# Optimization experiments

Hardware: AMD Instinct MI355X
Metric: run time of the kernel (lower is better)

## Reference

```python
import jax, jax.numpy as jnp
import numpy as np

ALPHA = 8.3  # depth-similarity decay from Depth-aware CNN
K = 3        # kernel size
PAD = 1      # padding (stride=1, dilation=1)


def _patches(x, k, pad):
    """Extract kxk stride-1 patches. x: (B,C,H,W) -> (B,C,k,k,H,W)."""
    B, C, H, W = x.shape
    xp = jnp.pad(x, ((0, 0), (0, 0), (pad, pad), (pad, pad)))
    rows = []
    for i in range(k):
        cols = [xp[:, :, i:i + H, j:j + W] for j in range(k)]
        rows.append(jnp.stack(cols, axis=2))          # (B,C,k,H,W)
    return jnp.stack(rows, axis=2)                     # (B,C,k,k,H,W)


def setup_inputs() -> dict:
    key = jax.random.key(0)
    k1, k2, k3 = jax.random.split(key, 3)
    B, Cin, H, W = 8, 512, 64, 64
    Cout = 64
    x = jax.random.normal(k1, (B, Cin, H, W), dtype=jnp.float32)
    depth = jax.random.uniform(k2, (B, 1, H, W), dtype=jnp.float32)
    stdv = 1.0 / np.sqrt(Cin * K * K)
    weight = jax.random.uniform(k3, (Cout, Cin, K, K), dtype=jnp.float32,
                                minval=-stdv, maxval=stdv)
    return {"input": x, "depth": depth, "weight": weight}


def reference(input, depth, weight):
    # depth-modulated conv: out(p0) = sum_pn w(pn) * x(p0+pn) * exp(-a*|d(p0)-d(p0+pn)|)
    xpat = _patches(input, K, PAD)                 # (B,Cin,K,K,H,W)
    dpat = _patches(depth, K, PAD)                 # (B,1,K,K,H,W)
    d0 = depth[:, :, None, None, :, :]             # center depth (B,1,1,1,H,W)
    gate = jnp.exp(-ALPHA * jnp.abs(d0 - dpat))    # (B,1,K,K,H,W)
    out = jnp.einsum('ocij,bcijhw->bohw', weight, xpat * gate)
    return out
```

## Files before the change

### kernel.cpp

```cpp
#include <hip/hip_runtime.h>
#include <math.h>

#define ALPHA 8.3f
#define XSZ   16896
#define WSZ   36864
#define BUFSZ 53760

typedef short v8s  __attribute__((ext_vector_type(8)));
typedef float v16f __attribute__((ext_vector_type(16)));
typedef float v4f  __attribute__((ext_vector_type(4)));

static __device__ __forceinline__ unsigned short f2bf(float f) {
    unsigned int u = __float_as_uint(f);
    u = (u + 0x7fffu + ((u >> 16) & 1u)) >> 16;
    return (unsigned short)u;
}

static __device__ __forceinline__ void async16(const void* g, void* l) {
    __builtin_amdgcn_global_load_lds(
        (const __attribute__((address_space(1))) unsigned int*)g,
        (__attribute__((address_space(3))) unsigned int*)l, 16, 0, 0);
}

__global__ __launch_bounds__(256) void prep_weights(const float* __restrict__ w,
                                                    unsigned short* __restrict__ wt) {
    const int i = blockIdx.x * 256 + threadIdx.x;
    if (i >= 294912) return;
    const int j    = i & 7;
    const int lane = (i >> 3) & 63;
    const int F    = i >> 9;
    const int kc   = F & 1;
    const int mt   = (F >> 1) & 1;
    const int tq   = F >> 2;
    const int tap  = tq % 9;
    const int ss   = tq / 9;
    const int o    = mt * 32 + (lane & 31);
    const int cin  = ss * 32 + kc * 16 + (lane >> 5) * 8 + j;
    wt[i] = f2bf(w[(o * 512 + cin) * 9 + tap]);
}

__global__ __launch_bounds__(384, 2)
void depthconv_v17(const float* __restrict__ x,
                   const float* __restrict__ depth,
                   const unsigned short* __restrict__ wt,
                   float* __restrict__ out) {
    __shared__ __align__(16) char smem[2 * BUFSZ];

    const int bx   = blockIdx.x;
    const int xcd  = bx & 7;
    const int i0   = bx >> 3;
    const int b    = i0 & 7;
    const int h0   = (xcd * 4 + (i0 >> 3)) * 2;

    const int tid  = threadIdx.x;
    const int wid  = tid >> 6;
    const int lane = tid & 63;
    const int l31  = lane & 31;
    const int half = lane >> 5;
    const int rt   = wid & 1;
    const int di   = wid >> 1;

    const float* xb = x + (size_t)b * 2097152;
    const float* xsrc[3];
    int  goff[3];
    bool gval[3], gact[3];
#pragma unroll
    for (int it = 0; it < 3; ++it) {
        const int g_i = it * 384 + tid;
        const bool act = (g_i < 1056);
        const int p_ = g_i / 264;
        const int s_ = g_i - p_ * 264;
        const int r_ = s_ / 66, c_ = s_ - r_ * 66;
        const int hh = h0 - 1 + r_, ww = c_ - 1;
        const bool val = act && hh >= 0 && hh < 64 && ww >= 0 && ww < 64;
        gact[it] = act;
        gval[it] = val;
        goff[it] = g_i * 16;
        xsrc[it] = val ? (xb + (size_t)(p_ * 8) * 4096 + hh * 64 + ww) : xb;
    }

#define XLOAD(SS, V)                                                             \
    {                                                                            \
        const size_t adv = (size_t)(SS) * 131072;       \
        _Pragma("unroll")                                                        \
        for (int it = 0; it < 3; ++it)                                           \
            _Pragma("unroll")                                                    \
            for (int e = 0; e < 8; ++e)                                          \
                V[it][e] = gval[it] ? xsrc[it][adv + (size_t)e * 4096] : 0.f;    \
    }
#define XWRITE(V, BSEL)                                                          \
    {                                                                            \
        char* dx = smem + (BSEL) * BUFSZ;                                        \
        _Pragma("unroll")                                                        \
        for (int it = 0; it < 3; ++it)                                           \
            if (gact[it]) {                                                      \
                uint4 u;                                                         \
                u.x = f2bf(V[it][0]) | ((unsigned)f2bf(V[it][1]) << 16);         \
                u.y = f2bf(V[it][2]) | ((unsigned)f2bf(V[it][3]) << 16);         \
                u.z = f2bf(V[it][4]) | ((unsigned)f2bf(V[it][5]) << 16);         \
                u.w = f2bf(V[it][6]) | ((unsigned)f2bf(V[it][7]) << 16);         \
                *(uint4*)(dx + goff[it]) = u;                                    \
            }                                                                    \
    }
#define WISSUE(SS, BSEL)                                                         \
    {                                                                            \
        char* dw = smem + (BSEL) * BUFSZ + XSZ;                                  \
        const char* ws = (const char*)wt + (size_t)(SS) * WSZ;                   \
        _Pragma("unroll")                                                        \
        for (int k = 0; k < 6; ++k)                                              \
            async16(ws + (size_t)(k * 384 + tid) * 16,                           \
                    dw + (k * 384 + tid) * 16);                                  \
    }

    float gt[2][3];
    {
        const float* dp = depth + (size_t)b * 4096;
        const int hq = h0 + rt;
        const int hn = hq + di - 1;
#pragma unroll
        for (int n = 0; n < 2; ++n) {
            const int wq = n * 32 + l31;
            const float d0 = dp[hq * 64 + wq];
#pragma unroll
            for (int dj = 0; dj < 3; ++dj) {
                const int wn = wq + dj - 1;
                const float dn = (hn >= 0 && hn < 64 && wn >= 0 && wn < 64)
                                     ? dp[hn * 64 + wn] : 0.f;
                gt[n][dj] = __expf(-ALPHA * fabsf(d0 - dn));
            }
        }
    }

    v16f a00[3], a01[3], a10[3], a11[3];
#pragma unroll
    for (int d = 0; d < 3; ++d)
#pragma unroll
        for (int r = 0; r < 16; ++r) { a00[d][r] = 0.f; a01[d][r] = 0.f;
                                       a10[d][r] = 0.f; a11[d][r] = 0.f; }

    const int aOff = XSZ + di * 12288 + lane * 16;
    const int bOff = (half * 264 + (rt + di) * 66 + l31) * 16;

    float v[3][8];
    WISSUE(0, 0);
    XLOAD(0, v);
    XWRITE(v, 0);

    for (int ss = 0; ss < 16; ++ss) {
        __syncthreads();
        const int cur = ss & 1;
        const int nxt = cur ^ 1;
        if (ss < 15) {
            WISSUE(ss + 1, nxt);
            XLOAD(ss + 1, v);
        }
        const char* ba = smem + cur * BUFSZ + aOff;
        const char* bb = smem + cur * BUFSZ + bOff;
#pragma unroll
        for (int dj = 0; dj < 3; ++dj) {
#pragma unroll
            for (int kc = 0; kc < 2; ++kc) {
                const v8s w0 = *(const v8s*)(ba + ((dj * 2 + 0) * 2 + kc) * 1024);
                const v8s w1 = *(const v8s*)(ba + ((dj * 2 + 1) * 2 + kc) * 1024);
                const v8s x0 = *(const v8s*)(bb + kc * 8448 + (0 * 32 + dj) * 16);
                const v8s x1 = *(const v8s*)(bb + kc * 8448 + (1 * 32 + dj) * 16);
                a00[dj] = __builtin_amdgcn_mfma_f32_32x32x16_bf16(w0, x0, a00[dj], 0, 0, 0);
                a01[dj] = __builtin_amdgcn_mfma_f32_32x32x16_bf16(w1, x0, a01[dj], 0, 0, 0);
                a10[dj] = __builtin_amdgcn_mfma_f32_32x32x16_bf16(w0, x1, a10[dj], 0, 0, 0);
                a11[dj] = __builtin_amdgcn_mfma_f32_32x32x16_bf16(w1, x1, a11[dj], 0, 0, 0);
            }
        }
        if (ss < 15) XWRITE(v, nxt);
    }

#pragma unroll
    for (int r = 0; r < 16; ++r) {
        a00[0][r] = gt[0][0] * a00[0][r];
        a00[0][r] = fmaf(gt[0][1], a00[1][r], a00[0][r]);
        a00[0][r] = fmaf(gt[0][2], a00[2][r], a00[0][r]);
        a01[0][r] = gt[0][0] * a01[0][r];
        a01[0][r] = fmaf(gt[0][1], a01[1][r], a01[0][r]);
        a01[0][r] = fmaf(gt[0][2], a01[2][r], a01[0][r]);
        a10[0][r] = gt[1][0] * a10[0][r];
        a10[0][r] = fmaf(gt[1][1], a10[1][r], a10[0][r]);
        a10[0][r] = fmaf(gt[1][2], a10[2][r], a10[0][r]);
        a11[0][r] = gt[1][0] * a11[0][r];
        a11[0][r] = fmaf(gt[1][1], a11[1][r], a11[0][r]);
        a11[0][r] = fmaf(gt[1][2], a11[2][r], a11[0][r]);
    }

    __syncthreads();
    float* red = (float*)smem;
    const int rbase = rt * 4096 + lane * 4;
#define EPI_STORE(ACC, N, MT)                                                    \
    _Pragma("unroll")                                                            \
    for (int qd = 0; qd < 4; ++qd) {                                             \
        v4f vv; vv[0] = ACC[0][qd * 4]; vv[1] = ACC[0][qd * 4 + 1];              \
        vv[2] = ACC[0][qd * 4 + 2]; vv[3] = ACC[0][qd * 4 + 3];                  \
        *(v4f*)&red[rbase + ((N) * 2 + (MT)) * 1024 + qd * 256] = vv;            \
    }
#define EPI_ADD(ACC, N, MT)                                                      \
    _Pragma("unroll")                                                            \
    for (int qd = 0; qd < 4; ++qd) {                                             \
        v4f vv = *(const v4f*)&red[rbase + ((N) * 2 + (MT)) * 1024 + qd * 256];  \
        vv[0] += ACC[0][qd * 4];     vv[1] += ACC[0][qd * 4 + 1];                \
        vv[2] += ACC[0][qd * 4 + 2]; vv[3] += ACC[0][qd * 4 + 3];                \
        *(v4f*)&red[rbase + ((N) * 2 + (MT)) * 1024 + qd * 256] = vv;            \
    }
    if (di == 2) {
        EPI_STORE(a00, 0, 0) EPI_STORE(a01, 0, 1) EPI_STORE(a10, 1, 0) EPI_STORE(a11, 1, 1)
    }
    __syncthreads();
    if (di == 1) {
        EPI_ADD(a00, 0, 0) EPI_ADD(a01, 0, 1) EPI_ADD(a10, 1, 0) EPI_ADD(a11, 1, 1)
    }
    __syncthreads();
    if (di == 0) {
        float* ob = out + (size_t)b * 262144 + (h0 + rt) * 64;
#define EPI_OUT(ACC, N, MT)                                                      \
    _Pragma("unroll")                                                            \
    for (int qd = 0; qd < 4; ++qd) {                                             \
        const v4f vv = *(const v4f*)&red[rbase + ((N) * 2 + (MT)) * 1024 + qd * 256]; \
        _Pragma("unroll")                                                        \
        for (int j = 0; j < 4; ++j) {                                            \
            const int rg = qd * 4 + j;                                           \
            const int o = (MT) * 32 + (rg & 3) + 8 * (rg >> 2) + 4 * half;       \
            ob[(size_t)o * 4096 + (N) * 32 + l31] = ACC[0][rg] + vv[j];          \
        }                                                                        \
    }
        EPI_OUT(a00, 0, 0) EPI_OUT(a01, 0, 1) EPI_OUT(a10, 1, 0) EPI_OUT(a11, 1, 1)
    }
}

extern "C" void kernel_launch(void* const* d_in, const int* in_sizes, int n_in,
                              void* d_out, int out_size, void* d_ws, size_t ws_size,
                              hipStream_t stream) {
    const float* x      = (const float*)d_in[0];
    const float* depth  = (const float*)d_in[1];
    const float* weight = (const float*)d_in[2];
    float* out = (float*)d_out;

    unsigned short* wtb = (unsigned short*)d_ws;

    prep_weights<<<1152, 256, 0, stream>>>(weight, wtb);
    depthconv_v17<<<256, 384, 0, stream>>>(x, depth, wtb, out);
}
```

Before: 133.6 us.

## Split output tiles in half width and halve K-chunk for higher occupancy

Each block now covers a 2x32 output tile instead of 2x64, doubling the grid to 512 blocks, and each pipeline stage takes 16 input channels instead of 32, so the loop runs 32 stages. This shrinks LDS buffers and accumulator registers, allowing 3 blocks per CU instead of 2, meant to improve latency hiding and fill the GPU better. In exchange, the x halo and the weights are reloaded by twice as many blocks, there are twice as many barriers, and each stage does fewer MFMAs.

```diff
diff --git a/kernel.cpp b/kernel.cpp
--- a/kernel.cpp
+++ b/kernel.cpp
@@ -2,9 +2,9 @@
 #include <math.h>
 
 #define ALPHA 8.3f
-#define XSZ   16896
-#define WSZ   36864
-#define BUFSZ 53760
+#define XSZ   4352
+#define WSZ   18432
+#define BUFSZ 22784
 
 typedef short v8s  __attribute__((ext_vector_type(8)));
 typedef float v16f __attribute__((ext_vector_type(16)));
@@ -29,18 +29,17 @@
     const int j    = i & 7;
     const int lane = (i >> 3) & 63;
     const int F    = i >> 9;
-    const int kc   = F & 1;
-    const int mt   = (F >> 1) & 1;
-    const int tq   = F >> 2;
-    const int tap  = tq % 9;
-    const int ss   = tq / 9;
+    const int mt   = F & 1;
+    const int t    = F >> 1;
+    const int tap  = t % 9;
+    const int ss   = t / 9;
     const int o    = mt * 32 + (lane & 31);
-    const int cin  = ss * 32 + kc * 16 + (lane >> 5) * 8 + j;
+    const int cin  = ss * 16 + (lane >> 5) * 8 + j;
     wt[i] = f2bf(w[(o * 512 + cin) * 9 + tap]);
 }
 
-__global__ __launch_bounds__(384, 2)
-void depthconv_v17(const float* __restrict__ x,
+__global__ __launch_bounds__(384, 3)
+void depthconv_v18(const float* __restrict__ x,
                    const float* __restrict__ depth,
                    const unsigned short* __restrict__ wt,
                    float* __restrict__ out) {
@@ -49,8 +48,10 @@
     const int bx   = blockIdx.x;
     const int xcd  = bx & 7;
     const int i0   = bx >> 3;
-    const int b    = i0 & 7;
-    const int h0   = (xcd * 4 + (i0 >> 3)) * 2;
+    const int wt2  = i0 & 1;
+    const int b    = (i0 >> 1) & 7;
+    const int ht   = xcd * 4 + (i0 >> 4);
+    const int h0   = ht * 2, w0 = wt2 * 32;
 
     const int tid  = threadIdx.x;
     const int wid  = tid >> 6;
@@ -61,96 +62,82 @@
     const int di   = wid >> 1;
 
     const float* xb = x + (size_t)b * 2097152;
-    const float* xsrc[3];
-    int  goff[3];
-    bool gval[3], gact[3];
-#pragma unroll
-    for (int it = 0; it < 3; ++it) {
-        const int g_i = it * 384 + tid;
-        const bool act = (g_i < 1056);
-        const int p_ = g_i / 264;
-        const int s_ = g_i - p_ * 264;
-        const int r_ = s_ / 66, c_ = s_ - r_ * 66;
-        const int hh = h0 - 1 + r_, ww = c_ - 1;
-        const bool val = act && hh >= 0 && hh < 64 && ww >= 0 && ww < 64;
-        gact[it] = act;
-        gval[it] = val;
-        goff[it] = g_i * 16;
-        xsrc[it] = val ? (xb + (size_t)(p_ * 8) * 4096 + hh * 64 + ww) : xb;
+
+    const bool xact = (tid < 272);
+    bool xval; int goff; const float* xsrc;
+    {
+        const int g  = xact ? tid : 0;
+        const int p_ = (g >= 136) ? 1 : 0;
+        const int s_ = g - p_ * 136;
+        const int r_ = s_ / 34, c_ = s_ - r_ * 34;
+        const int hh = h0 - 1 + r_, ww = w0 - 1 + c_;
+        xval = xact && hh >= 0 && hh < 64 && ww >= 0 && ww < 64;
+        goff = g * 16;
+        xsrc = xval ? (xb + (size_t)(p_ * 8) * 4096 + hh * 64 + ww) : xb;
     }
 
 #define XLOAD(SS, V)                                                             \
     {                                                                            \
-        const size_t adv = (size_t)(SS) * 131072;       \
+        const size_t adv = (size_t)(SS) * 65536;                                 \
         _Pragma("unroll")                                                        \
-        for (int it = 0; it < 3; ++it)                                           \
-            _Pragma("unroll")                                                    \
-            for (int e = 0; e < 8; ++e)                                          \
-                V[it][e] = gval[it] ? xsrc[it][adv + (size_t)e * 4096] : 0.f;    \
+        for (int e = 0; e < 8; ++e)                                              \
+            V[e] = xval ? xsrc[adv + (size_t)e * 4096] : 0.f;                    \
     }
 #define XWRITE(V, BSEL)                                                          \
     {                                                                            \
-        char* dx = smem + (BSEL) * BUFSZ;                                        \
-        _Pragma("unroll")                                                        \
-        for (int it = 0; it < 3; ++it)                                           \
-            if (gact[it]) {                                                      \
-                uint4 u;                                                         \
-                u.x = f2bf(V[it][0]) | ((unsigned)f2bf(V[it][1]) << 16);         \
-                u.y = f2bf(V[it][2]) | ((unsigned)f2bf(V[it][3]) << 16);         \
-                u.z = f2bf(V[it][4]) | ((unsigned)f2bf(V[it][5]) << 16);         \
-                u.w = f2bf(V[it][6]) | ((unsigned)f2bf(V[it][7]) << 16);         \
-                *(uint4*)(dx + goff[it]) = u;                                    \
-            }                                                                    \
+        if (xact) {                                                              \
+            uint4 u;                                                             \
+            u.x = f2bf(V[0]) | ((unsigned)f2bf(V[1]) << 16);                     \
+            u.y = f2bf(V[2]) | ((unsigned)f2bf(V[3]) << 16);                     \
+            u.z = f2bf(V[4]) | ((unsigned)f2bf(V[5]) << 16);                     \
+            u.w = f2bf(V[6]) | ((unsigned)f2bf(V[7]) << 16);                     \
+            *(uint4*)(smem + (BSEL) * BUFSZ + goff) = u;                         \
+        }                                                                        \
     }
 #define WISSUE(SS, BSEL)                                                         \
     {                                                                            \
         char* dw = smem + (BSEL) * BUFSZ + XSZ;                                  \
         const char* ws = (const char*)wt + (size_t)(SS) * WSZ;                   \
         _Pragma("unroll")                                                        \
-        for (int k = 0; k < 6; ++k)                                              \
+        for (int k = 0; k < 3; ++k)                                              \
             async16(ws + (size_t)(k * 384 + tid) * 16,                           \
                     dw + (k * 384 + tid) * 16);                                  \
     }
 
-    float gt[2][3];
+    float gt[3];
     {
         const float* dp = depth + (size_t)b * 4096;
-        const int hq = h0 + rt;
+        const int hq = h0 + rt, wq = w0 + l31;
         const int hn = hq + di - 1;
-#pragma unroll
-        for (int n = 0; n < 2; ++n) {
-            const int wq = n * 32 + l31;
-            const float d0 = dp[hq * 64 + wq];
-#pragma unroll
-            for (int dj = 0; dj < 3; ++dj) {
-                const int wn = wq + dj - 1;
-                const float dn = (hn >= 0 && hn < 64 && wn >= 0 && wn < 64)
-                                     ? dp[hn * 64 + wn] : 0.f;
-                gt[n][dj] = __expf(-ALPHA * fabsf(d0 - dn));
-            }
+        const float d0 = dp[hq * 64 + wq];
+#pragma unroll
+        for (int dj = 0; dj < 3; ++dj) {
+            const int wn = wq + dj - 1;
+            const float dn = (hn >= 0 && hn < 64 && wn >= 0 && wn < 64)
+                                 ? dp[hn * 64 + wn] : 0.f;
+            gt[dj] = __expf(-ALPHA * fabsf(d0 - dn));
         }
     }
 
-    v16f a00[3], a01[3], a10[3], a11[3];
+    v16f am0[3], am1[3];
 #pragma unroll
     for (int d = 0; d < 3; ++d)
 #pragma unroll
-        for (int r = 0; r < 16; ++r) { a00[d][r] = 0.f; a01[d][r] = 0.f;
-                                       a10[d][r] = 0.f; a11[d][r] = 0.f; }
-
-    const int aOff = XSZ + di * 12288 + lane * 16;
-    const int bOff = (half * 264 + (rt + di) * 66 + l31) * 16;
-
-    float v[3][8];
+        for (int r = 0; r < 16; ++r) { am0[d][r] = 0.f; am1[d][r] = 0.f; }
+
+    const int aOff = XSZ + (di * 6) * 1024 + lane * 16;
+    const int bOff = (half * 136 + (rt + di) * 34 + l31) * 16;
+
+    float v[8];
     WISSUE(0, 0);
     XLOAD(0, v);
     XWRITE(v, 0);
 
-    for (int ss = 0; ss < 16; ++ss) {
+    for (int ss = 0; ss < 32; ++ss) {
         __syncthreads();
         const int cur = ss & 1;
         const int nxt = cur ^ 1;
-        if (ss < 15) {
+        if (ss < 31) {
             WISSUE(ss + 1, nxt);
             XLOAD(ss + 1, v);
         }
@@ -158,77 +145,63 @@
         const char* bb = smem + cur * BUFSZ + bOff;
 #pragma unroll
         for (int dj = 0; dj < 3; ++dj) {
-#pragma unroll
-            for (int kc = 0; kc < 2; ++kc) {
-                const v8s w0 = *(const v8s*)(ba + ((dj * 2 + 0) * 2 + kc) * 1024);
-                const v8s w1 = *(const v8s*)(ba + ((dj * 2 + 1) * 2 + kc) * 1024);
-                const v8s x0 = *(const v8s*)(bb + kc * 8448 + (0 * 32 + dj) * 16);
-                const v8s x1 = *(const v8s*)(bb + kc * 8448 + (1 * 32 + dj) * 16);
-                a00[dj] = __builtin_amdgcn_mfma_f32_32x32x16_bf16(w0, x0, a00[dj], 0, 0, 0);
-                a01[dj] = __builtin_amdgcn_mfma_f32_32x32x16_bf16(w1, x0, a01[dj], 0, 0, 0);
-                a10[dj] = __builtin_amdgcn_mfma_f32_32x32x16_bf16(w0, x1, a10[dj], 0, 0, 0);
-                a11[dj] = __builtin_amdgcn_mfma_f32_32x32x16_bf16(w1, x1, a11[dj], 0, 0, 0);
-            }
+            const v8s w0v = *(const v8s*)(ba + (dj * 2 + 0) * 1024);
+            const v8s w1v = *(const v8s*)(ba + (dj * 2 + 1) * 1024);
+            const v8s xv  = *(const v8s*)(bb + dj * 16);
+            am0[dj] = __builtin_amdgcn_mfma_f32_32x32x16_bf16(w0v, xv, am0[dj], 0, 0, 0);
+            am1[dj] = __builtin_amdgcn_mfma_f32_32x32x16_bf16(w1v, xv, am1[dj], 0, 0, 0);
         }
-        if (ss < 15) XWRITE(v, nxt);
-    }
-
+        if (ss < 31) XWRITE(v, nxt);
+    }
+
+    float m0[16], m1[16];
 #pragma unroll
     for (int r = 0; r < 16; ++r) {
-        a00[0][r] = gt[0][0] * a00[0][r];
-        a00[0][r] = fmaf(gt[0][1], a00[1][r], a00[0][r]);
-        a00[0][r] = fmaf(gt[0][2], a00[2][r], a00[0][r]);
-        a01[0][r] = gt[0][0] * a01[0][r];
-        a01[0][r] = fmaf(gt[0][1], a01[1][r], a01[0][r]);
-        a01[0][r] = fmaf(gt[0][2], a01[2][r], a01[0][r]);
-        a10[0][r] = gt[1][0] * a10[0][r];
-        a10[0][r] = fmaf(gt[1][1], a10[1][r], a10[0][r]);
-        a10[0][r] = fmaf(gt[1][2], a10[2][r], a10[0][r]);
-        a11[0][r] = gt[1][0] * a11[0][r];
-        a11[0][r] = fmaf(gt[1][1], a11[1][r], a11[0][r]);
-        a11[0][r] = fmaf(gt[1][2], a11[2][r], a11[0][r]);
+        m0[r] = gt[0] * am0[0][r];
+        m0[r] = fmaf(gt[1], am0[1][r], m0[r]);
+        m0[r] = fmaf(gt[2], am0[2][r], m0[r]);
+        m1[r] = gt[0] * am1[0][r];
+        m1[r] = fmaf(gt[1], am1[1][r], m1[r]);
+        m1[r] = fmaf(gt[2], am1[2][r], m1[r]);
     }
 
     __syncthreads();
     float* red = (float*)smem;
-    const int rbase = rt * 4096 + lane * 4;
-#define EPI_STORE(ACC, N, MT)                                                    \
+    const int rb0 = (0 * 2 + rt) * 1024 + lane * 4;
+    const int rb1 = (1 * 2 + rt) * 1024 + lane * 4;
+#define EPI_STORE(M, RB)                                                         \
     _Pragma("unroll")                                                            \
     for (int qd = 0; qd < 4; ++qd) {                                             \
-        v4f vv; vv[0] = ACC[0][qd * 4]; vv[1] = ACC[0][qd * 4 + 1];              \
-        vv[2] = ACC[0][qd * 4 + 2]; vv[3] = ACC[0][qd * 4 + 3];                  \
-        *(v4f*)&red[rbase + ((N) * 2 + (MT)) * 1024 + qd * 256] = vv;            \
-    }
-#define EPI_ADD(ACC, N, MT)                                                      \
+        v4f vv; vv[0] = M[qd * 4]; vv[1] = M[qd * 4 + 1];                        \
+        vv[2] = M[qd * 4 + 2]; vv[3] = M[qd * 4 + 3];                            \
+        *(v4f*)&red[(RB) + qd * 256] = vv;                                       \
+    }
+#define EPI_ADD(M, RB)                                                           \
     _Pragma("unroll")                                                            \
     for (int qd = 0; qd < 4; ++qd) {                                             \
-        v4f vv = *(const v4f*)&red[rbase + ((N) * 2 + (MT)) * 1024 + qd * 256];  \
-        vv[0] += ACC[0][qd * 4];     vv[1] += ACC[0][qd * 4 + 1];                \
-        vv[2] += ACC[0][qd * 4 + 2]; vv[3] += ACC[0][qd * 4 + 3];                \
-        *(v4f*)&red[rbase + ((N) * 2 + (MT)) * 1024 + qd * 256] = vv;            \
-    }
-    if (di == 2) {
-        EPI_STORE(a00, 0, 0) EPI_STORE(a01, 0, 1) EPI_STORE(a10, 1, 0) EPI_STORE(a11, 1, 1)
-    }
+        v4f vv = *(const v4f*)&red[(RB) + qd * 256];                             \
+        vv[0] += M[qd * 4];     vv[1] += M[qd * 4 + 1];                          \
+        vv[2] += M[qd * 4 + 2]; vv[3] += M[qd * 4 + 3];                          \
+        *(v4f*)&red[(RB) + qd * 256] = vv;                                       \
+    }
+    if (di == 2) { EPI_STORE(m0, rb0) EPI_STORE(m1, rb1) }
     __syncthreads();
-    if (di == 1) {
-        EPI_ADD(a00, 0, 0) EPI_ADD(a01, 0, 1) EPI_ADD(a10, 1, 0) EPI_ADD(a11, 1, 1)
-    }
+    if (di == 1) { EPI_ADD(m0, rb0) EPI_ADD(m1, rb1) }
     __syncthreads();
     if (di == 0) {
-        float* ob = out + (size_t)b * 262144 + (h0 + rt) * 64;
-#define EPI_OUT(ACC, N, MT)                                                      \
+        float* ob = out + (size_t)b * 262144 + (h0 + rt) * 64 + w0;
+#define EPI_OUT(M, RB, MT)                                                       \
     _Pragma("unroll")                                                            \
     for (int qd = 0; qd < 4; ++qd) {                                             \
-        const v4f vv = *(const v4f*)&red[rbase + ((N) * 2 + (MT)) * 1024 + qd * 256]; \
+        const v4f vv = *(const v4f*)&red[(RB) + qd * 256];                       \
         _Pragma("unroll")                                                        \
         for (int j = 0; j < 4; ++j) {                                            \
             const int rg = qd * 4 + j;                                           \
             const int o = (MT) * 32 + (rg & 3) + 8 * (rg >> 2) + 4 * half;       \
-            ob[(size_t)o * 4096 + (N) * 32 + l31] = ACC[0][rg] + vv[j];          \
+            ob[(size_t)o * 4096 + l31] = M[rg] + vv[j];                          \
         }                                                                        \
     }
-        EPI_OUT(a00, 0, 0) EPI_OUT(a01, 0, 1) EPI_OUT(a10, 1, 0) EPI_OUT(a11, 1, 1)
+        EPI_OUT(m0, rb0, 0) EPI_OUT(m1, rb1, 1)
     }
 }
 
@@ -243,5 +216,5 @@
     unsigned short* wtb = (unsigned short*)d_ws;
 
     prep_weights<<<1152, 256, 0, stream>>>(weight, wtb);
-    depthconv_v17<<<256, 384, 0, stream>>>(x, depth, wtb, out);
-}
+    depthconv_v18<<<512, 384, 0, stream>>>(x, depth, wtb, out);
+}
```

New measurement: 152.9 us. 14.5% more time.
